# Kernel tuning notes

Hardware: AMD Instinct MI355X
Metric: run time of the kernel (lower is better)

## Reference

```python
import jax, jax.numpy as jnp
import numpy as np

TRANSFER_VOLUME = 0.1
KW = 1e-14  # water ion product
LN10 = float(np.log(10.0))


def binarize_weight(w):
    # clip to [-1,1], forward pass is sign(), gradient flows through the clip (STE)
    clipped = jnp.clip(w, -1.0, 1.0)
    rounded = jnp.sign(clipped)
    return clipped + jax.lax.stop_gradient(rounded - clipped)


def setup_inputs() -> dict:
    key = jax.random.key(0)
    kx, kw = jax.random.split(key)
    batch, n_in, n_out = 4096, 4096, 4096
    x = jax.random.uniform(kx, (batch, n_in), dtype=jnp.float32)
    w = jax.random.normal(kw, (n_in, n_out), dtype=jnp.float32)
    return {"x": x, "w": w}


def reference(x, w):
    binary_weights = binarize_weight(w)  # [n_in, n_out], values in {-1, 0, +1}
    input_sz = x.shape[1]
    input_h_conc = 10.0 ** (-x)                       # [B, n_in]
    input_oh_conc = KW / input_h_conc                  # [B, n_in]
    input_h_num_moles = input_h_conc * TRANSFER_VOLUME
    input_oh_num_moles = input_oh_conc * TRANSFER_VOLUME
    acid_moles_sum = input_h_num_moles @ binary_weights   # [B, n_out]
    base_moles_sum = input_oh_num_moles @ binary_weights  # [B, n_out]
    remaining_moles = acid_moles_sum - base_moles_sum
    acid_is_limiting = remaining_moles < 0
    remaining_moles_conc = jnp.abs(remaining_moles) / (input_sz * TRANSFER_VOLUME)
    resultant_h_conc = jnp.where(acid_is_limiting, KW / remaining_moles_conc, remaining_moles_conc)
    resultant_ph = -jnp.log(resultant_h_conc) / LN10
    return resultant_ph
```

## Files before the change

### kernel.cpp

```cpp
#include <hip/hip_runtime.h>
#include <math.h>

#define BATCH 4096
#define NIN   4096
#define NOUT  4096

typedef __attribute__((ext_vector_type(8))) short bf16x8;
typedef __attribute__((ext_vector_type(8))) unsigned short u16x8;
typedef __attribute__((ext_vector_type(4))) float f32x4;

__device__ __forceinline__ float2 compute_terms(float xv) {
    float h  = (float)exp10(-(double)xv);
    float oh = 1e-14f / h;
    return make_float2(h * 0.1f, oh * 0.1f);
}
__device__ __forceinline__ unsigned short bf16_rne(float v) {
    unsigned int b = __float_as_uint(v);
    return (unsigned short)((b + 0x7FFFu + ((b >> 16) & 1u)) >> 16);
}
__device__ __forceinline__ float signf_of(float wv) {
    return (wv > 0.f) ? 1.f : ((wv < 0.f) ? -1.f : 0.f);
}
__device__ __forceinline__ unsigned short signbf16_of(float wv) {
    return (wv > 0.f) ? 0x3F80u : ((wv < 0.f) ? 0xBF80u : 0u);
}

#define GLOAD16(g, l)                                                        \
    __builtin_amdgcn_global_load_lds(                                        \
        (const __attribute__((address_space(1))) void*)(g),                  \
        (__attribute__((address_space(3))) void*)(l), 16, 0, 0)

__global__ __launch_bounds__(256) void precompute_all(const float* __restrict__ x,
                                                      const float* __restrict__ w,
                                                      float* __restrict__ aaT,
                                                      unsigned short* __restrict__ ab,
                                                      unsigned short* __restrict__ sT,
                                                      unsigned short* __restrict__ sP) {
    const int tid = threadIdx.x;
    if (blockIdx.y < 64) {
        __shared__ float tile[64][65];
        const int m0 = blockIdx.y * 64, k0 = blockIdx.x * 64;
        #pragma unroll
        for (int it = 0; it < 4; ++it) {
            int idx = tid + it * 256;
            int row = idx >> 4, q = idx & 15;
            float4 xv = *(const float4*)(x + (size_t)(m0 + row) * NIN + k0 + q * 4);
            float2 t0 = compute_terms(xv.x), t1 = compute_terms(xv.y),
                   t2 = compute_terms(xv.z), t3 = compute_terms(xv.w);
            *(ushort4*)(ab + (size_t)(m0 + row) * NIN + k0 + q * 4) =
                make_ushort4(bf16_rne(t0.y), bf16_rne(t1.y), bf16_rne(t2.y), bf16_rne(t3.y));
            tile[row][q * 4 + 0] = t0.x; tile[row][q * 4 + 1] = t1.x;
            tile[row][q * 4 + 2] = t2.x; tile[row][q * 4 + 3] = t3.x;
        }
        __syncthreads();
        #pragma unroll
        for (int it = 0; it < 4; ++it) {
            int idx = tid + it * 256;
            int krow = idx >> 4, q = idx & 15;
            float4 v = make_float4(tile[q * 4 + 0][krow], tile[q * 4 + 1][krow],
                                   tile[q * 4 + 2][krow], tile[q * 4 + 3][krow]);
            *(float4*)(aaT + (size_t)(k0 + krow) * NIN + m0 + q * 4) = v;
        }
    } else {
        __shared__ unsigned short tileu[64][68];
        const int k0 = (blockIdx.y - 64) * 64, n0 = blockIdx.x * 64;
        #pragma unroll
        for (int it = 0; it < 4; ++it) {
            int idx = tid + it * 256;
            int krow = idx >> 4, q = idx & 15;
            float4 wv = *(const float4*)(w + (size_t)(k0 + krow) * NOUT + n0 + q * 4);
            ushort4 sg = make_ushort4(signbf16_of(wv.x), signbf16_of(wv.y),
                                      signbf16_of(wv.z), signbf16_of(wv.w));
            *(ushort4*)&tileu[krow][q * 4] = sg;
            int c0  = n0 + q * 4;
            int grp = c0 >> 7, wi = c0 & 127;
            int pos = grp * 128 + ((wi & 63) >> 2) * 8 + ((wi >> 6) & 1) * 4;
            *(ushort4*)(sP + (size_t)(k0 + krow) * NOUT + pos) = sg;
        }
        __syncthreads();
        #pragma unroll
        for (int it = 0; it < 2; ++it) {
            int idx = tid + it * 256;
            int n = idx >> 3, kc = idx & 7;
            u16x8 v;
            #pragma unroll
            for (int j = 0; j < 8; ++j) v[j] = tileu[kc * 8 + j][n];
            *(u16x8*)(sT + (size_t)(n0 + n) * NIN + k0 + kc * 8) = v;
        }
    }
}

__global__ __launch_bounds__(256, 3) void acid_base_fused(const float* __restrict__ AaT,
                                                          const unsigned short* __restrict__ SignP,
                                                          const unsigned short* __restrict__ Ab,
                                                          const unsigned short* __restrict__ SignT,
                                                          float* __restrict__ out) {
    __shared__ __align__(16) char smem[34816];
    float (*As)[16][128]          = (float (*)[16][128])smem;
    unsigned short (*BsU)[16][128] = (unsigned short (*)[16][128])(smem + 16384);
    float (*BoutH)[68]            = (float (*)[68])smem;

    const int tid = threadIdx.x;
    const int tx  = tid & 15;
    const int ty  = tid >> 4;
    const int w   = tid >> 6;
    const int l   = tid & 63;
    const int g   = l >> 4;
    const int r16 = l & 15;
    const int bm0 = blockIdx.y * 128;
    const int bn0 = blockIdx.x * 128;

    const int lrow = (l >> 5);
    const int lcol = (l & 31) * 4;
    const int brow = l >> 4;
    const int bcol = (l & 15) * 8;

    float ma[8][8] = {}, ca[8][8] = {};

    #define AISSUE(s, b)                                                            \
        {                                                                           \
            const int k0_ = (s) * 16;                                               \
            _Pragma("unroll")                                                       \
            for (int j = 0; j < 2; ++j) {                                           \
                const int kr_ = w * 4 + 2 * j;                                      \
                GLOAD16(AaT + (size_t)(k0_ + kr_ + lrow) * NIN + bm0 + lcol,        \
                        &As[b][kr_][0]);                                            \
            }                                                                       \
            GLOAD16(SignP + (size_t)(k0_ + w * 4 + brow) * NOUT + bn0 + bcol,       \
                    &BsU[b][w * 4][0]);                                             \
        }

    #define ACOMP(s, b)                                                             \
        {                                                                           \
            _Pragma("unroll 4")                                                     \
            for (int k = 0; k < 16; ++k) {                                          \
                const float4 pa = *(const float4*)&As[b][k][ty * 8];                \
                const float4 pb = *(const float4*)&As[b][k][ty * 8 + 4];            \
                const uint4  su = *(const uint4*)&BsU[b][k][tx * 8];                \
                const float av[8] = {pa.x, pa.y, pa.z, pa.w, pb.x, pb.y, pb.z, pb.w};\
                const float sn[8] = {                                               \
                    __uint_as_float(su.x << 16), __uint_as_float(su.x & 0xFFFF0000u),\
                    __uint_as_float(su.y << 16), __uint_as_float(su.y & 0xFFFF0000u),\
                    __uint_as_float(su.z << 16), __uint_as_float(su.z & 0xFFFF0000u),\
                    __uint_as_float(su.w << 16), __uint_as_float(su.w & 0xFFFF0000u)};\
                _Pragma("unroll")                                                   \
                for (int m = 0; m < 8; ++m)                                         \
                    _Pragma("unroll")                                               \
                    for (int n = 0; n < 8; ++n)                                     \
                        ca[m][n] = fmaf(av[m], sn[n], ca[m][n]);                    \
            }                                                                       \
            if ((((s) + 1) & 31) == 0) {                                            \
                _Pragma("unroll")                                                   \
                for (int m = 0; m < 8; ++m)                                         \
                    _Pragma("unroll")                                               \
                    for (int n = 0; n < 8; ++n) {                                   \
                        ma[m][n] += ca[m][n]; ca[m][n] = 0.f;                       \
                    }                                                               \
            }                                                                       \
        }

    AISSUE(0, 0);
    __syncthreads();

    for (int s2 = 0; s2 < 128; ++s2) {
        const int s = 2 * s2;
        AISSUE(s + 1, 1);
        ACOMP(s, 0);
        __syncthreads();
        if (s + 2 < 256) AISSUE(s + 2, 0);
        ACOMP(s + 1, 1);
        __syncthreads();
    }

    f32x4 acc[2][8] = {};
    {
        const unsigned short* a0 = Ab + (size_t)(bm0 + w * 32 + r16) * NIN + g * 8;
        const unsigned short* a1 = Ab + (size_t)(bm0 + w * 32 + 16 + r16) * NIN + g * 8;
        #pragma unroll 4
        for (int s = 0; s < 128; ++s) {
            const int k0 = s * 32;
            bf16x8 af0 = *(const bf16x8*)(a0 + k0);
            bf16x8 af1 = *(const bf16x8*)(a1 + k0);
            #pragma unroll
            for (int tc = 0; tc < 8; ++tc) {
                bf16x8 bf = *(const bf16x8*)(SignT + (size_t)(bn0 + tc * 16 + r16) * NIN + k0 + g * 8);
                acc[0][tc] = __builtin_amdgcn_mfma_f32_16x16x32_bf16(af0, bf, acc[0][tc], 0, 0, 0);
                acc[1][tc] = __builtin_amdgcn_mfma_f32_16x16x32_bf16(af1, bf, acc[1][tc], 0, 0, 0);
            }
        }
    }

    __syncthreads();
    #pragma unroll
    for (int hh = 0; hh < 2; ++hh) {
        #pragma unroll
        for (int tr = 0; tr < 2; ++tr)
            #pragma unroll
            for (int tc = 0; tc < 4; ++tc)
                #pragma unroll
                for (int rr = 0; rr < 4; ++rr)
                    BoutH[w * 32 + tr * 16 + g * 4 + rr][tc * 16 + r16] = acc[tr][hh * 4 + tc][rr];
        __syncthreads();
        #pragma unroll
        for (int m = 0; m < 8; ++m) {
            const int row = ty * 8 + m;
            const float4 bv = *(const float4*)&BoutH[row][tx * 4];
            const float bb[4] = {bv.x, bv.y, bv.z, bv.w};
            float ph[4];
            #pragma unroll
            for (int n = 0; n < 4; ++n) {
                float r    = ma[m][hh * 4 + n] - bb[n];
                float conc = fabsf(r) / 409.6f;
                float hc   = (r < 0.f) ? (1e-14f / conc) : conc;
                ph[n]      = (-logf(hc)) / 2.302585092994046f;
            }
            *(float4*)(out + (size_t)(bm0 + row) * NOUT + bn0 + hh * 64 + tx * 4) =
                make_float4(ph[0], ph[1], ph[2], ph[3]);
        }
        __syncthreads();
    }
    #undef AISSUE
    #undef ACOMP
}

__global__ __launch_bounds__(256, 2) void acid_gemm_fly(const float* __restrict__ X,
                                                        const float* __restrict__ W,
                                                        float* __restrict__ out) {
    __shared__ float2 Asf[32][128 + 2];
    __shared__ float  Bsf[32][64];
    const int tid = threadIdx.x;
    const int tx = tid & 15, ty = tid >> 4;
    const int bm0 = blockIdx.y * 128, bn0 = blockIdx.x * 64;
    float ma[8][4] = {}, mb[8][4] = {}, ca[8][4] = {}, cb[8][4] = {};
    for (int s = 0; s < 128; ++s) {
        const int k0 = s * 32;
        for (int idx = tid; idx < 128 * 32; idx += 256) {
            int m = idx >> 5, k = idx & 31;
            Asf[k][m] = compute_terms(X[(size_t)(bm0 + m) * NIN + k0 + k]);
        }
        for (int idx = tid; idx < 32 * 64; idx += 256) {
            int k = idx >> 6, c = idx & 63;
            Bsf[k][c] = signf_of(W[(size_t)(k0 + k) * NOUT + bn0 + c]);
        }
        __syncthreads();
        #pragma unroll 4
        for (int k = 0; k < 32; ++k) {
            float2 av[8]; float sv[4];
            #pragma unroll
            for (int m = 0; m < 8; ++m) av[m] = Asf[k][ty * 8 + m];
            #pragma unroll
            for (int n = 0; n < 4; ++n) sv[n] = Bsf[k][tx * 4 + n];
            #pragma unroll
            for (int m = 0; m < 8; ++m)
                #pragma unroll
                for (int n = 0; n < 4; ++n) {
                    ca[m][n] = fmaf(av[m].x, sv[n], ca[m][n]);
                    cb[m][n] = fmaf(av[m].y, sv[n], cb[m][n]);
                }
        }
        if (((s + 1) & 15) == 0) {
            #pragma unroll
            for (int m = 0; m < 8; ++m)
                #pragma unroll
                for (int n = 0; n < 4; ++n) {
                    ma[m][n] += ca[m][n]; ca[m][n] = 0.f;
                    mb[m][n] += cb[m][n]; cb[m][n] = 0.f;
                }
        }
        __syncthreads();
    }
    #pragma unroll
    for (int m = 0; m < 8; ++m) {
        int row = bm0 + ty * 8 + m;
        #pragma unroll
        for (int n = 0; n < 4; ++n) {
            int col = bn0 + tx * 4 + n;
            float r = ma[m][n] - mb[m][n];
            float conc = fabsf(r) / 409.6f;
            float hc = (r < 0.f) ? (1e-14f / conc) : conc;
            out[(size_t)row * NOUT + col] = (-logf(hc)) / 2.302585092994046f;
        }
    }
}

extern "C" void kernel_launch(void* const* d_in, const int* in_sizes, int n_in,
                              void* d_out, int out_size, void* d_ws, size_t ws_size,
                              hipStream_t stream) {
    const float* x = (const float*)d_in[0];
    const float* w = (const float*)d_in[1];
    float* out = (float*)d_out;

    const size_t nElem = (size_t)BATCH * NIN;
    float*          aaT   = (float*)d_ws;
    unsigned short* ab    = (unsigned short*)((char*)d_ws + nElem * 4);
    unsigned short* signT = (unsigned short*)((char*)d_ws + nElem * 6);
    unsigned short* signP = (unsigned short*)((char*)d_ws + nElem * 8);

    if (ws_size >= nElem * 10) {
        precompute_all <<<dim3(64, 128), 256, 0, stream>>>(x, w, aaT, ab, signT, signP);
        acid_base_fused<<<dim3(32, 32), 256, 0, stream>>>(aaT, signP, ab, signT, out);
    } else {
        acid_gemm_fly<<<dim3(NOUT / 64, BATCH / 128), dim3(256), 0, stream>>>(x, w, out);
    }
}
```

Baseline: 2.085 ms.

## Give each wave private LDS tiles and replace block barriers with wave waits

The fp32 sign-GEMM stage now has each wave stage its own 32-row slice of A and its own full copy of the B sign tile in a private LDS region. This lets the two block-wide __syncthreads per iteration be replaced by a per-wave s_waitcnt, so waves no longer stall on each other. The cost is four times more global/L2 traffic for B, since every wave loads the same tile, and LDS use grows from 34 KB to 48 KB per block, which puts pressure on the requested occupancy of three blocks per CU.

After: 2.071 ms. Within noise of the previous version (-0.7%).

```diff
diff --git a/kernel.cpp b/kernel.cpp
--- a/kernel.cpp
+++ b/kernel.cpp
@@ -95,10 +95,7 @@
                                                           const unsigned short* __restrict__ Ab,
                                                           const unsigned short* __restrict__ SignT,
                                                           float* __restrict__ out) {
-    __shared__ __align__(16) char smem[34816];
-    float (*As)[16][128]          = (float (*)[16][128])smem;
-    unsigned short (*BsU)[16][128] = (unsigned short (*)[16][128])(smem + 16384);
-    float (*BoutH)[68]            = (float (*)[68])smem;
+    __shared__ __align__(16) char smem[49152];
 
     const int tid = threadIdx.x;
     const int tx  = tid & 15;
@@ -107,13 +104,13 @@
     const int l   = tid & 63;
     const int g   = l >> 4;
     const int r16 = l & 15;
+    const int ty3 = ty & 3;
     const int bm0 = blockIdx.y * 128;
     const int bn0 = blockIdx.x * 128;
 
-    const int lrow = (l >> 5);
-    const int lcol = (l & 31) * 4;
-    const int brow = l >> 4;
-    const int bcol = (l & 15) * 8;
+    float*        asf = (float*)(smem + w * 4096);
+    unsigned int* bsu = (unsigned int*)(smem + 16384 + w * 8192);
+    float (*BoutH)[68] = (float (*)[68])smem;
 
     float ma[8][8] = {}, ca[8][8] = {};
 
@@ -121,22 +118,24 @@
         {                                                                           \
             const int k0_ = (s) * 16;                                               \
             _Pragma("unroll")                                                       \
-            for (int j = 0; j < 2; ++j) {                                           \
-                const int kr_ = w * 4 + 2 * j;                                      \
-                GLOAD16(AaT + (size_t)(k0_ + kr_ + lrow) * NIN + bm0 + lcol,        \
-                        &As[b][kr_][0]);                                            \
-            }                                                                       \
-            GLOAD16(SignP + (size_t)(k0_ + w * 4 + brow) * NOUT + bn0 + bcol,       \
-                    &BsU[b][w * 4][0]);                                             \
+            for (int j = 0; j < 2; ++j)                                             \
+                GLOAD16(AaT + (size_t)(k0_ + j * 8 + (l >> 3)) * NIN                \
+                            + bm0 + w * 32 + (l & 7) * 4,                           \
+                        (char*)asf + (b) * 2048 + j * 1024);                        \
+            _Pragma("unroll")                                                       \
+            for (int j = 0; j < 4; ++j)                                             \
+                GLOAD16(SignP + (size_t)(k0_ + j * 4 + (l >> 4)) * NOUT             \
+                              + bn0 + (l & 15) * 8,                                 \
+                        (char*)bsu + (b) * 4096 + j * 1024);                        \
         }
 
     #define ACOMP(s, b)                                                             \
         {                                                                           \
             _Pragma("unroll 4")                                                     \
             for (int k = 0; k < 16; ++k) {                                          \
-                const float4 pa = *(const float4*)&As[b][k][ty * 8];                \
-                const float4 pb = *(const float4*)&As[b][k][ty * 8 + 4];            \
-                const uint4  su = *(const uint4*)&BsU[b][k][tx * 8];                \
+                const float4 pa = *(const float4*)(asf + (b) * 512 + k * 32 + ty3 * 8);\
+                const float4 pb = *(const float4*)(asf + (b) * 512 + k * 32 + ty3 * 8 + 4);\
+                const uint4  su = *(const uint4*)(bsu + (b) * 1024 + k * 64 + tx * 4);\
                 const float av[8] = {pa.x, pa.y, pa.z, pa.w, pb.x, pb.y, pb.z, pb.w};\
                 const float sn[8] = {                                               \
                     __uint_as_float(su.x << 16), __uint_as_float(su.x & 0xFFFF0000u),\
@@ -159,17 +158,16 @@
             }                                                                       \
         }
 
+    #define WAVE_WAIT() asm volatile("s_waitcnt vmcnt(0) lgkmcnt(0)" ::: "memory")
+
     AISSUE(0, 0);
-    __syncthreads();
-
-    for (int s2 = 0; s2 < 128; ++s2) {
-        const int s = 2 * s2;
-        AISSUE(s + 1, 1);
-        ACOMP(s, 0);
-        __syncthreads();
-        if (s + 2 < 256) AISSUE(s + 2, 0);
-        ACOMP(s + 1, 1);
-        __syncthreads();
+    WAVE_WAIT();
+
+    for (int s = 0; s < 256; ++s) {
+        const int b = s & 1;
+        if (s + 1 < 256) AISSUE(s + 1, b ^ 1);
+        ACOMP(s, b);
+        WAVE_WAIT();
     }
 
     f32x4 acc[2][8] = {};
@@ -221,6 +219,7 @@
     }
     #undef AISSUE
     #undef ACOMP
+    #undef WAVE_WAIT
 }
 
 __global__ __launch_bounds__(256, 2) void acid_gemm_fly(const float* __restrict__ X,
```
